# Performance work log

Measured on AMD Instinct MI355X. Metric: run time of the kernel, lower is better.

## Reference

```python
import jax, jax.numpy as jnp
import numpy as np

H = 23
Wd = 23
P = H * Wd            # 529 positions per 23x23 score map (hard-coded in the torch module)
B = 16384             # batch of score maps
TH = 0.05             # init kwarg peak_th
KS = 5                # init kwarg ks (max-pool kernel)
BN_EPS = 1e-5


def setup_inputs() -> dict:
    key = jax.random.key(0)
    k = jax.random.split(key, 18)
    def n(i, shape, scale=1.0):
        return scale * jax.random.normal(k[i], shape, dtype=jnp.float32)
    return {
        "target_scores": n(0, (2, B, P)),
        "anno_label": jax.random.uniform(k[1], (1, B, P), dtype=jnp.float32),
        # Conv1d(2->8, k=1) == Linear(2->8); BatchNorm1d in eval mode (running stats)
        "W1": n(2, (8, 2), 0.5), "b1": n(3, (8,), 0.1),
        "g1": 1.0 + n(4, (8,), 0.1), "be1": n(5, (8,), 0.1),
        "m1": n(6, (8,), 0.1), "v1": jax.random.uniform(k[7], (8,), minval=0.5, maxval=1.5),
        "W2": n(8, (8, 8), 0.3), "b2": n(9, (8,), 0.1),
        "g2": 1.0 + n(10, (8,), 0.1), "be2": n(11, (8,), 0.1),
        "m2": n(12, (8,), 0.1), "v2": jax.random.uniform(k[13], (8,), minval=0.5, maxval=1.5),
        "W3": n(14, (1, 8), 0.3), "b3": n(15, (1,), 0.1),
    }


def _find_peaks(scores_flat):
    """find_local_maxima: maxpool(ks, stride 1, pad ks//2) equality + threshold,
    then sort peaks by descending intensity per batch. Fixed-size padded version:
    returns coords [B,P,2] (float), sorted scores [B,P], valid mask [B,P]."""
    s = scores_flat.reshape(-1, H, Wd)
    smax = jax.lax.reduce_window(s, -jnp.inf, jax.lax.max, (1, KS, KS), (1, 1, 1), "SAME")
    mask = ((s == smax) & (s > TH)).reshape(-1, P)
    order = jnp.argsort(-jnp.where(mask, scores_flat, -jnp.inf), axis=1)
    sorted_s = jnp.take_along_axis(scores_flat, order, axis=1)
    valid = jnp.take_along_axis(mask, order, axis=1)
    coords = jnp.stack([(order // Wd).astype(jnp.float32),
                        (order % Wd).astype(jnp.float32)], axis=-1)
    return coords, sorted_s, valid


def _bn(x, g, b, m, v):
    return (x - m) * (g / jnp.sqrt(v + BN_EPS)) + b


def reference(target_scores, anno_label, W1, b1, g1, be1, m1, v1,
              W2, b2, g2, be2, m2, v2, W3, b3):
    scores_old = target_scores[0]            # [B,P]
    scores_cur = target_scores[1]            # [B,P]
    y_old = anno_label[0]                    # [B,P]

    c_old, s_old, val_old = _find_peaks(scores_old)
    c_cur, s_cur, val_cur = _find_peaks(scores_cur)

    # dcf.max2d(train_y_old): argmax coordinate of the training label
    gidx = jnp.argmax(y_old, axis=1)
    gc = jnp.stack([gidx // Wd, gidx % Wd], axis=-1).astype(jnp.float32)   # [B,2]

    # nearest old peak to the ground-truth coordinate
    d2 = jnp.sum((gc[:, None, :] - c_old) ** 2, axis=-1)
    d2 = jnp.where(val_old, d2, jnp.inf)
    pidx = jnp.argmin(d2, axis=1)
    cg = c_old[jnp.arange(c_old.shape[0]), pidx]                           # [B,2]

    # f_old = sum_j s_j * (cg - c_j) over valid old peaks
    sm_old = jnp.where(val_old, s_old, 0.0)
    f_old = jnp.sum(sm_old, axis=1)[:, None] * cg - jnp.einsum("bp,bpd->bd", sm_old, c_old)

    # f_cur[j] = sum_k s_k * (c_j - c_k)  (closed form of the pairwise sum)
    sm_cur = jnp.where(val_cur, s_cur, 0.0)
    S_cur = jnp.sum(sm_cur, axis=1)                                        # [B]
    M_cur = jnp.einsum("bp,bpd->bd", sm_cur, c_cur)                        # [B,2]
    f_cur = S_cur[:, None, None] * c_cur - M_cur[:, None, :]               # [B,P,2]

    diff2 = jnp.sum((f_old[:, None, :] - f_cur) ** 2, axis=-1)
    err = jnp.sqrt(jnp.maximum(diff2, 1e-24))                              # [B,P]

    feats = jnp.stack([err, s_cur], axis=-1)                               # [B,P,2]
    h = jax.nn.relu(_bn(feats @ W1.T + b1, g1, be1, m1, v1))
    h = jax.nn.relu(_bn(h @ W2.T + b2, g2, be2, m2, v2))
    pred = (h @ W3.T + b3)[..., 0]                                         # [B,P]
    pred = jnp.where(val_cur, pred, 0.0)  # only real peaks carry predictions
    return pred, c_cur, s_cur, val_cur
```

## Files before the change

kernel.cpp:

```cpp
#include <hip/hip_runtime.h>
#include <math.h>

#define H_   23
#define W_   23
#define P_   529
#define TH_  0.05f
#define NC   9
#define CAP  96
#define WPB  4
#define NTHR (WPB * 64)
#define WFLO (2 * P_ + 112)

#define WSYNC() do { asm volatile("" ::: "memory"); __builtin_amdgcn_wave_barrier(); } while (0)

__global__ __launch_bounds__(NTHR, 8) void peak_kernel(
    const float* __restrict__ tscores,
    const float* __restrict__ anno,
    const float* __restrict__ W1, const float* __restrict__ b1,
    const float* __restrict__ g1, const float* __restrict__ be1,
    const float* __restrict__ m1, const float* __restrict__ v1,
    const float* __restrict__ W2, const float* __restrict__ b2,
    const float* __restrict__ g2, const float* __restrict__ be2,
    const float* __restrict__ m2, const float* __restrict__ v2,
    const float* __restrict__ W3, const float* __restrict__ b3,
    float* __restrict__ out, int B)
{
    const int t  = threadIdx.x;
    const int l  = t & 63;
    const int wv = t >> 6;
    const int b  = blockIdx.x * WPB + wv;

    __shared__ float lds[WPB * WFLO];
    float* m  = lds + wv * WFLO;
    float* r  = m + P_;
    float* wt = r + P_;
    float* cs = r;
    int*   cp = (int*)(r + CAP);
    int*   rk = (int*)(r + 2*CAP);
    int*   ri = (int*)r;
    float* ps = wt;

    const unsigned long long ltm = (1ull << l) - 1ull;

    {
        int o = l >> 3;
        float sc2o = g2[o] / sqrtf(v2[o] + 1e-5f);
        wt[24 + l] = W2[l] * sc2o;
        if (l < 8) {
            float sc1 = g1[l] / sqrtf(v1[l] + 1e-5f);
            wt[2*l]     = W1[2*l] * sc1;
            wt[2*l + 1] = W1[2*l + 1] * sc1;
            wt[16 + l]  = (b1[l] - m1[l]) * sc1 + be1[l];
            float sc2 = g2[l] / sqrtf(v2[l] + 1e-5f);
            wt[88 + l]  = (b2[l] - m2[l]) * sc2 + be2[l];
            wt[96 + l]  = W3[l];
            if (l == 0) wt[104] = b3[0];
        }
    }

    const float* yrow = anno + (size_t)b * P_;
    const float* sold = tscores + (size_t)b * P_;
    const float* scur = tscores + (size_t)B * P_ + (size_t)b * P_;
    float ao[NC], so[NC], sc[NC];
    #pragma unroll
    for (int c = 0; c < NC; c++) { int p = 64*c + l; ao[c] = (p < P_) ? yrow[p] : -INFINITY; }
    #pragma unroll
    for (int c = 0; c < NC; c++) { int p = 64*c + l; so[c] = (p < P_) ? sold[p] : 0.f; }
    #pragma unroll
    for (int c = 0; c < NC; c++) { int p = 64*c + l; sc[c] = (p < P_) ? scur[p] : 0.f; }

    float bv = -INFINITY; int bi = 0x7fffffff;
    #pragma unroll
    for (int c = 0; c < NC; c++) {
        int p = 64*c + l;
        if (p < P_ && ao[c] > bv) { bv = ao[c]; bi = p; }
    }
    #pragma unroll
    for (int d = 32; d > 0; d >>= 1) {
        float ov = __shfl_xor(bv, d); int oi = __shfl_xor(bi, d);
        if (ov > bv || (ov == bv && oi < bi)) { bv = ov; bi = oi; }
    }
    const int gy = bi / W_, gx = bi - (bi / W_) * W_;

    #pragma unroll
    for (int c = 0; c < NC; c++) { int p = 64*c + l; if (p < P_) m[p] = so[c]; }
    WSYNC();
    #pragma unroll
    for (int c = 0; c < NC; c++) {
        int p = 64*c + l;
        if (p < P_) {
            int y = p / W_, x = p - y * W_;
            const float* row = &m[y * W_];
            float mx = row[x];
            if (x >= 1)      mx = fmaxf(mx, row[x-1]);
            if (x >= 2)      mx = fmaxf(mx, row[x-2]);
            if (x <= W_-2)   mx = fmaxf(mx, row[x+1]);
            if (x <= W_-3)   mx = fmaxf(mx, row[x+2]);
            r[p] = mx;
        }
    }
    WSYNC();
    float So = 0.f, Mor = 0.f, Moc = 0.f;
    float nd2 = INFINITY, ns = -INFINITY; int np = 0;
    #pragma unroll
    for (int c = 0; c < NC; c++) {
        int p = 64*c + l;
        if (p < P_) {
            int y = p / W_, x = p - y * W_;
            float s = so[c];
            float sm = r[p];
            if (y >= 1)    sm = fmaxf(sm, r[p - W_]);
            if (y >= 2)    sm = fmaxf(sm, r[p - 2*W_]);
            if (y <= H_-2) sm = fmaxf(sm, r[p + W_]);
            if (y <= H_-3) sm = fmaxf(sm, r[p + 2*W_]);
            if (s == sm && s > TH_) {
                So += s; Mor += s * (float)y; Moc += s * (float)x;
                int dy = gy - y, dx = gx - x;
                float d2 = (float)(dy*dy + dx*dx);
                if (d2 < nd2 || (d2 == nd2 && (s > ns || (s == ns && p < np)))) {
                    nd2 = d2; ns = s; np = p;
                }
            }
        }
    }
    #pragma unroll
    for (int d = 32; d > 0; d >>= 1) {
        So += __shfl_xor(So, d); Mor += __shfl_xor(Mor, d); Moc += __shfl_xor(Moc, d);
        float od2 = __shfl_xor(nd2, d), os = __shfl_xor(ns, d); int op = __shfl_xor(np, d);
        if (od2 < nd2 || (od2 == nd2 && (os > ns || (os == ns && op < np)))) {
            nd2 = od2; ns = os; np = op;
        }
    }
    const int cy = np / W_, cx = np - (np / W_) * W_;
    const float foldr = So * (float)cy - Mor;
    const float foldc = So * (float)cx - Moc;

    WSYNC();
    #pragma unroll
    for (int c = 0; c < NC; c++) { int p = 64*c + l; if (p < P_) m[p] = sc[c]; }
    WSYNC();
    #pragma unroll
    for (int c = 0; c < NC; c++) {
        int p = 64*c + l;
        if (p < P_) {
            int y = p / W_, x = p - y * W_;
            const float* row = &m[y * W_];
            float mx = row[x];
            if (x >= 1)      mx = fmaxf(mx, row[x-1]);
            if (x >= 2)      mx = fmaxf(mx, row[x-2]);
            if (x <= W_-2)   mx = fmaxf(mx, row[x+1]);
            if (x <= W_-3)   mx = fmaxf(mx, row[x+2]);
            r[p] = mx;
        }
    }
    WSYNC();
    float Sc = 0.f, Mcr = 0.f, Mcc = 0.f;
    int vb = 0;
    #pragma unroll
    for (int c = 0; c < NC; c++) {
        int p = 64*c + l;
        if (p < P_) {
            int y = p / W_, x = p - y * W_;
            float s = sc[c];
            float sm = r[p];
            if (y >= 1)    sm = fmaxf(sm, r[p - W_]);
            if (y >= 2)    sm = fmaxf(sm, r[p - 2*W_]);
            if (y <= H_-2) sm = fmaxf(sm, r[p + W_]);
            if (y <= H_-3) sm = fmaxf(sm, r[p + 2*W_]);
            if (s == sm && s > TH_) {
                vb |= 1 << c;
                Sc += s; Mcr += s * (float)y; Mcc += s * (float)x;
            }
        }
    }
    #pragma unroll
    for (int d = 32; d > 0; d >>= 1) {
        Sc += __shfl_xor(Sc, d); Mcr += __shfl_xor(Mcr, d); Mcc += __shfl_xor(Mcc, d);
    }
    WSYNC();

    int K = 0;
    int nb[NC];
    #pragma unroll
    for (int c = 0; c < NC; c++) {
        bool v = (vb >> c) & 1;
        unsigned long long bt = __ballot(v);
        int my = K + __popcll(bt & ltm);
        nb[c] = my;
        if (v && my < CAP) { cs[my] = sc[c]; cp[my] = 64*c + l; }
        K += __popcll(bt);
    }
    WSYNC();

    const int Kc = K > CAP ? CAP : K;
    for (int i = l; i < Kc; i += 64) {
        float si = cs[i]; int pi = cp[i]; int rr = 0;
        for (int j = 0; j < Kc; j++) {
            float sj = cs[j]; int pj = cp[j];
            rr += (sj > si || (sj == si && pj < pi)) ? 1 : 0;
        }
        rk[i] = rr;
    }
    WSYNC();

    auto mlp = [&](int i, float& pv, int& rko) {
        int p = cp[i];
        float s = cs[i];
        rko = rk[i];
        int y = p / W_, x = p - (p / W_) * W_;
        float fcr = Sc * (float)y - Mcr;
        float fcc = Sc * (float)x - Mcc;
        float dr = foldr - fcr, dc = foldc - fcc;
        float err = sqrtf(fmaxf(dr*dr + dc*dc, 1e-24f));
        float h1[8];
        #pragma unroll
        for (int o = 0; o < 8; o++)
            h1[o] = fmaxf(fmaf(err, wt[2*o], fmaf(s, wt[2*o+1], wt[16+o])), 0.f);
        float pred = wt[104];
        #pragma unroll
        for (int o = 0; o < 8; o++) {
            float z = wt[88 + o];
            #pragma unroll
            for (int i2 = 0; i2 < 8; i2++) z = fmaf(h1[i2], wt[24 + o*8 + i2], z);
            pred = fmaf(fmaxf(z, 0.f), wt[96 + o], pred);
        }
        pv = pred;
    };
    float pv0 = 0.f, pv1 = 0.f; int rk0 = -1, rk1 = -1;
    if (l < Kc)      mlp(l, pv0, rk0);
    if (64 + l < Kc) mlp(64 + l, pv1, rk1);
    WSYNC();
    if (rk0 >= 0 && rk0 < CAP) ps[rk0] = pv0;
    if (rk1 >= 0 && rk1 < CAP) ps[rk1] = pv1;

    int slot[NC];
    #pragma unroll
    for (int c = 0; c < NC; c++) {
        int p = 64*c + l;
        if (p < P_) {
            bool v = (vb >> c) & 1;
            int n = nb[c];
            slot[c] = v ? ((n < CAP) ? rk[n] : n) : (K + p - n);
        }
    }
    WSYNC();
    #pragma unroll
    for (int c = 0; c < NC; c++) {
        int p = 64*c + l;
        if (p < P_) ri[slot[c]] = p;
    }
    WSYNC();

    const size_t BP = (size_t)B * P_;
    float* out_pred = out;
    float* out_c    = out + BP;
    float* out_s    = out + 3 * BP;
    float* out_v    = out + 4 * BP;
    const size_t rowbase = (size_t)b * P_;

    #pragma unroll
    for (int c = 0; c < NC; c++) {
        int j = 64*c + l;
        if (j < P_) {
            int p = ri[j];
            int y = p / W_, x = p - (p / W_) * W_;
            bool val = j < K;
            float pv = (val && j < CAP) ? ps[j] : 0.f;
            float s  = m[p];
            out_pred[rowbase + j] = pv;
            ((float2*)out_c)[rowbase + j] = make_float2((float)y, (float)x);
            out_s[rowbase + j] = s;
            out_v[rowbase + j] = val ? 1.f : 0.f;
        }
    }
}

extern "C" void kernel_launch(void* const* d_in, const int* in_sizes, int n_in,
                              void* d_out, int out_size, void* d_ws, size_t ws_size,
                              hipStream_t stream) {
    const int B = in_sizes[0] / (2 * P_);
    hipLaunchKernelGGL(peak_kernel, dim3((B + WPB - 1) / WPB), dim3(NTHR), 0, stream,
        (const float*)d_in[0], (const float*)d_in[1],
        (const float*)d_in[2], (const float*)d_in[3], (const float*)d_in[4],
        (const float*)d_in[5], (const float*)d_in[6], (const float*)d_in[7],
        (const float*)d_in[8], (const float*)d_in[9], (const float*)d_in[10],
        (const float*)d_in[11], (const float*)d_in[12], (const float*)d_in[13],
        (const float*)d_in[14], (const float*)d_in[15],
        (float*)d_out, B);
}
```

Measured before the change: 71.37 us.

## Pad max-pool staging with -inf borders, precompute folded MLP weights, nontemporal stores

```diff
diff --git a/kernel.cpp b/kernel.cpp
--- a/kernel.cpp
+++ b/kernel.cpp
@@ -9,13 +9,13 @@
 #define CAP  96
 #define WPB  4
 #define NTHR (WPB * 64)
-#define WFLO (2 * P_ + 112)
+#define WFLO 1248
+
+typedef float f2_t __attribute__((ext_vector_type(2)));
 
 #define WSYNC() do { asm volatile("" ::: "memory"); __builtin_amdgcn_wave_barrier(); } while (0)
 
-__global__ __launch_bounds__(NTHR, 8) void peak_kernel(
-    const float* __restrict__ tscores,
-    const float* __restrict__ anno,
+__global__ __launch_bounds__(64) void fold_kernel(
     const float* __restrict__ W1, const float* __restrict__ b1,
     const float* __restrict__ g1, const float* __restrict__ be1,
     const float* __restrict__ m1, const float* __restrict__ v1,
@@ -23,38 +23,56 @@
     const float* __restrict__ g2, const float* __restrict__ be2,
     const float* __restrict__ m2, const float* __restrict__ v2,
     const float* __restrict__ W3, const float* __restrict__ b3,
+    float* __restrict__ wf)
+{
+    const int l = threadIdx.x;
+    {
+        int o = l >> 3;
+        wf[24 + l] = W2[l] * (g2[o] / sqrtf(v2[o] + 1e-5f));
+    }
+    if (l < 8) {
+        float sc1 = g1[l] / sqrtf(v1[l] + 1e-5f);
+        wf[2*l]     = W1[2*l] * sc1;
+        wf[2*l + 1] = W1[2*l + 1] * sc1;
+        wf[16 + l]  = (b1[l] - m1[l]) * sc1 + be1[l];
+        float sc2 = g2[l] / sqrtf(v2[l] + 1e-5f);
+        wf[88 + l]  = (b2[l] - m2[l]) * sc2 + be2[l];
+        wf[96 + l]  = W3[l];
+        if (l == 0) wf[104] = b3[0];
+    }
+}
+
+__global__ __launch_bounds__(NTHR, 8) void peak_kernel(
+    const float* __restrict__ tscores,
+    const float* __restrict__ anno,
+    const float* __restrict__ wf,
     float* __restrict__ out, int B)
 {
     const int t  = threadIdx.x;
     const int l  = t & 63;
     const int wv = t >> 6;
     const int b  = blockIdx.x * WPB + wv;
+    if (b >= B) return;
 
     __shared__ float lds[WPB * WFLO];
-    float* m  = lds + wv * WFLO;
-    float* r  = m + P_;
-    float* wt = r + P_;
-    float* cs = r;
-    int*   cp = (int*)(r + CAP);
-    int*   rk = (int*)(r + 2*CAP);
-    int*   ri = (int*)r;
-    float* ps = wt;
+    float* m27 = lds + wv * WFLO;
+    float* r27 = m27 + 621;
+    float* cs  = r27;
+    int*   cp  = (int*)(r27 + CAP);
+    int*   rk  = (int*)(r27 + 2*CAP);
+    int*   ri  = (int*)r27;
+    float* ps  = r27 + 529;
 
     const unsigned long long ltm = (1ull << l) - 1ull;
 
-    {
-        int o = l >> 3;
-        float sc2o = g2[o] / sqrtf(v2[o] + 1e-5f);
-        wt[24 + l] = W2[l] * sc2o;
-        if (l < 8) {
-            float sc1 = g1[l] / sqrtf(v1[l] + 1e-5f);
-            wt[2*l]     = W1[2*l] * sc1;
-            wt[2*l + 1] = W1[2*l + 1] * sc1;
-            wt[16 + l]  = (b1[l] - m1[l]) * sc1 + be1[l];
-            float sc2 = g2[l] / sqrtf(v2[l] + 1e-5f);
-            wt[88 + l]  = (b2[l] - m2[l]) * sc2 + be2[l];
-            wt[96 + l]  = W3[l];
-            if (l == 0) wt[104] = b3[0];
+    #pragma unroll
+    for (int k0 = 0; k0 < 2; k0++) {
+        int k = 64 * k0 + l;
+        if (k < 92) {
+            int rw = k >> 2, csel = k & 3;
+            m27[rw * 27 + csel + (csel >= 2 ? 23 : 0)] = -INFINITY;
+            int rsel = k / 23, col = k - 23 * (k / 23);
+            r27[(rsel + (rsel >= 2 ? 23 : 0)) * 23 + col] = -INFINITY;
         }
     }
 
@@ -69,6 +87,14 @@
     #pragma unroll
     for (int c = 0; c < NC; c++) { int p = 64*c + l; sc[c] = (p < P_) ? scur[p] : 0.f; }
 
+    int yy[NC], xx[NC];
+    #pragma unroll
+    for (int c = 0; c < NC; c++) {
+        int p = 64*c + l;
+        yy[c] = p / W_;
+        xx[c] = p - yy[c] * W_;
+    }
+
     float bv = -INFINITY; int bi = 0x7fffffff;
     #pragma unroll
     for (int c = 0; c < NC; c++) {
@@ -82,23 +108,34 @@
     }
     const int gy = bi / W_, gx = bi - (bi / W_) * W_;
 
-    #pragma unroll
-    for (int c = 0; c < NC; c++) { int p = 64*c + l; if (p < P_) m[p] = so[c]; }
-    WSYNC();
-    #pragma unroll
-    for (int c = 0; c < NC; c++) {
-        int p = 64*c + l;
-        if (p < P_) {
-            int y = p / W_, x = p - y * W_;
-            const float* row = &m[y * W_];
-            float mx = row[x];
-            if (x >= 1)      mx = fmaxf(mx, row[x-1]);
-            if (x >= 2)      mx = fmaxf(mx, row[x-2]);
-            if (x <= W_-2)   mx = fmaxf(mx, row[x+1]);
-            if (x <= W_-3)   mx = fmaxf(mx, row[x+2]);
-            r[p] = mx;
-        }
-    }
+    auto stage = [&](const float* v) {
+        #pragma unroll
+        for (int c = 0; c < NC; c++) {
+            int p = 64*c + l;
+            if (p < P_) m27[p + 4*yy[c] + 2] = v[c];
+        }
+    };
+    auto rowmax = [&]() {
+        #pragma unroll
+        for (int c = 0; c < NC; c++) {
+            int p = 64*c + l;
+            if (p < P_) {
+                const float* bp = &m27[p + 4*yy[c]];
+                float t0 = bp[0], t1 = bp[1], t2 = bp[2], t3 = bp[3], t4 = bp[4];
+                r27[p + 46] = fmaxf(fmaxf(fmaxf(t0, t1), fmaxf(t2, t3)), t4);
+            }
+        }
+    };
+    auto colmax = [&](int c) {
+        int p = 64*c + l;
+        const float* bp = &r27[p];
+        float t0 = bp[0], t1 = bp[23], t2 = bp[46], t3 = bp[69], t4 = bp[92];
+        return fmaxf(fmaxf(fmaxf(t0, t1), fmaxf(t2, t3)), t4);
+    };
+
+    stage(so);
+    WSYNC();
+    rowmax();
     WSYNC();
     float So = 0.f, Mor = 0.f, Moc = 0.f;
     float nd2 = INFINITY, ns = -INFINITY; int np = 0;
@@ -106,16 +143,12 @@
     for (int c = 0; c < NC; c++) {
         int p = 64*c + l;
         if (p < P_) {
-            int y = p / W_, x = p - y * W_;
             float s = so[c];
-            float sm = r[p];
-            if (y >= 1)    sm = fmaxf(sm, r[p - W_]);
-            if (y >= 2)    sm = fmaxf(sm, r[p - 2*W_]);
-            if (y <= H_-2) sm = fmaxf(sm, r[p + W_]);
-            if (y <= H_-3) sm = fmaxf(sm, r[p + 2*W_]);
+            float sm = colmax(c);
             if (s == sm && s > TH_) {
-                So += s; Mor += s * (float)y; Moc += s * (float)x;
-                int dy = gy - y, dx = gx - x;
+                float fy = (float)yy[c], fx = (float)xx[c];
+                So += s; Mor += s * fy; Moc += s * fx;
+                int dy = gy - yy[c], dx = gx - xx[c];
                 float d2 = (float)(dy*dy + dx*dx);
                 if (d2 < nd2 || (d2 == nd2 && (s > ns || (s == ns && p < np)))) {
                     nd2 = d2; ns = s; np = p;
@@ -136,23 +169,9 @@
     const float foldc = So * (float)cx - Moc;
 
     WSYNC();
-    #pragma unroll
-    for (int c = 0; c < NC; c++) { int p = 64*c + l; if (p < P_) m[p] = sc[c]; }
-    WSYNC();
-    #pragma unroll
-    for (int c = 0; c < NC; c++) {
-        int p = 64*c + l;
-        if (p < P_) {
-            int y = p / W_, x = p - y * W_;
-            const float* row = &m[y * W_];
-            float mx = row[x];
-            if (x >= 1)      mx = fmaxf(mx, row[x-1]);
-            if (x >= 2)      mx = fmaxf(mx, row[x-2]);
-            if (x <= W_-2)   mx = fmaxf(mx, row[x+1]);
-            if (x <= W_-3)   mx = fmaxf(mx, row[x+2]);
-            r[p] = mx;
-        }
-    }
+    stage(sc);
+    WSYNC();
+    rowmax();
     WSYNC();
     float Sc = 0.f, Mcr = 0.f, Mcc = 0.f;
     int vb = 0;
@@ -160,16 +179,11 @@
     for (int c = 0; c < NC; c++) {
         int p = 64*c + l;
         if (p < P_) {
-            int y = p / W_, x = p - y * W_;
             float s = sc[c];
-            float sm = r[p];
-            if (y >= 1)    sm = fmaxf(sm, r[p - W_]);
-            if (y >= 2)    sm = fmaxf(sm, r[p - 2*W_]);
-            if (y <= H_-2) sm = fmaxf(sm, r[p + W_]);
-            if (y <= H_-3) sm = fmaxf(sm, r[p + 2*W_]);
+            float sm = colmax(c);
             if (s == sm && s > TH_) {
                 vb |= 1 << c;
-                Sc += s; Mcr += s * (float)y; Mcc += s * (float)x;
+                Sc += s; Mcr += s * (float)yy[c]; Mcc += s * (float)xx[c];
             }
         }
     }
@@ -215,23 +229,22 @@
         float h1[8];
         #pragma unroll
         for (int o = 0; o < 8; o++)
-            h1[o] = fmaxf(fmaf(err, wt[2*o], fmaf(s, wt[2*o+1], wt[16+o])), 0.f);
-        float pred = wt[104];
+            h1[o] = fmaxf(fmaf(err, wf[2*o], fmaf(s, wf[2*o+1], wf[16+o])), 0.f);
+        float pred = wf[104];
         #pragma unroll
         for (int o = 0; o < 8; o++) {
-            float z = wt[88 + o];
+            float z = wf[88 + o];
             #pragma unroll
-            for (int i2 = 0; i2 < 8; i2++) z = fmaf(h1[i2], wt[24 + o*8 + i2], z);
-            pred = fmaf(fmaxf(z, 0.f), wt[96 + o], pred);
+            for (int i2 = 0; i2 < 8; i2++) z = fmaf(h1[i2], wf[24 + o*8 + i2], z);
+            pred = fmaf(fmaxf(z, 0.f), wf[96 + o], pred);
         }
         pv = pred;
     };
     float pv0 = 0.f, pv1 = 0.f; int rk0 = -1, rk1 = -1;
     if (l < Kc)      mlp(l, pv0, rk0);
     if (64 + l < Kc) mlp(64 + l, pv1, rk1);
-    WSYNC();
-    if (rk0 >= 0 && rk0 < CAP) ps[rk0] = pv0;
-    if (rk1 >= 0 && rk1 < CAP) ps[rk1] = pv1;
+    if (rk0 >= 0) ps[rk0] = pv0;
+    if (rk1 >= 0) ps[rk1] = pv1;
 
     int slot[NC];
     #pragma unroll
@@ -266,11 +279,12 @@
             int y = p / W_, x = p - (p / W_) * W_;
             bool val = j < K;
             float pv = (val && j < CAP) ? ps[j] : 0.f;
-            float s  = m[p];
-            out_pred[rowbase + j] = pv;
-            ((float2*)out_c)[rowbase + j] = make_float2((float)y, (float)x);
-            out_s[rowbase + j] = s;
-            out_v[rowbase + j] = val ? 1.f : 0.f;
+            float s  = m27[p + 4*y + 2];
+            f2_t co; co.x = (float)y; co.y = (float)x;
+            __builtin_nontemporal_store(pv, &out_pred[rowbase + j]);
+            __builtin_nontemporal_store(co, &((f2_t*)out_c)[rowbase + j]);
+            __builtin_nontemporal_store(s, &out_s[rowbase + j]);
+            __builtin_nontemporal_store(val ? 1.f : 0.f, &out_v[rowbase + j]);
         }
     }
 }
@@ -279,12 +293,14 @@
                               void* d_out, int out_size, void* d_ws, size_t ws_size,
                               hipStream_t stream) {
     const int B = in_sizes[0] / (2 * P_);
-    hipLaunchKernelGGL(peak_kernel, dim3((B + WPB - 1) / WPB), dim3(NTHR), 0, stream,
-        (const float*)d_in[0], (const float*)d_in[1],
+    float* wf = (float*)d_ws;
+    hipLaunchKernelGGL(fold_kernel, dim3(1), dim3(64), 0, stream,
         (const float*)d_in[2], (const float*)d_in[3], (const float*)d_in[4],
         (const float*)d_in[5], (const float*)d_in[6], (const float*)d_in[7],
         (const float*)d_in[8], (const float*)d_in[9], (const float*)d_in[10],
         (const float*)d_in[11], (const float*)d_in[12], (const float*)d_in[13],
-        (const float*)d_in[14], (const float*)d_in[15],
+        (const float*)d_in[14], (const float*)d_in[15], wf);
+    hipLaunchKernelGGL(peak_kernel, dim3((B + WPB - 1) / WPB), dim3(NTHR), 0, stream,
+        (const float*)d_in[0], (const float*)d_in[1], (const float*)wf,
         (float*)d_out, B);
 }
```

Result: slower. 106.3 us (+48.9%).

## Process two positions per lane with vectorized loads and direct global row-max

Applied to the files above, without the earlier changes.

```diff
diff --git a/kernel.cpp b/kernel.cpp
--- a/kernel.cpp
+++ b/kernel.cpp
@@ -6,10 +6,14 @@
 #define P_   529
 #define TH_  0.05f
 #define NC   9
+#define PC   5
 #define CAP  96
 #define WPB  4
 #define NTHR (WPB * 64)
-#define WFLO (2 * P_ + 112)
+#define WFLO 1176
+
+typedef float f2_t  __attribute__((ext_vector_type(2)));
+typedef float f2u_t __attribute__((ext_vector_type(2), aligned(4)));
 
 #define WSYNC() do { asm volatile("" ::: "memory"); __builtin_amdgcn_wave_barrier(); } while (0)
 
@@ -29,11 +33,12 @@
     const int l  = t & 63;
     const int wv = t >> 6;
     const int b  = blockIdx.x * WPB + wv;
+    if (b >= B) return;
 
     __shared__ float lds[WPB * WFLO];
-    float* m  = lds + wv * WFLO;
-    float* r  = m + P_;
-    float* wt = r + P_;
+    float* r  = lds + wv * WFLO;
+    float* m  = r + 532;
+    float* wt = r + 1064;
     float* cs = r;
     int*   cp = (int*)(r + CAP);
     int*   rk = (int*)(r + 2*CAP);
@@ -61,14 +66,10 @@
     const float* yrow = anno + (size_t)b * P_;
     const float* sold = tscores + (size_t)b * P_;
     const float* scur = tscores + (size_t)B * P_ + (size_t)b * P_;
-    float ao[NC], so[NC], sc[NC];
+
+    float ao[NC];
     #pragma unroll
     for (int c = 0; c < NC; c++) { int p = 64*c + l; ao[c] = (p < P_) ? yrow[p] : -INFINITY; }
-    #pragma unroll
-    for (int c = 0; c < NC; c++) { int p = 64*c + l; so[c] = (p < P_) ? sold[p] : 0.f; }
-    #pragma unroll
-    for (int c = 0; c < NC; c++) { int p = 64*c + l; sc[c] = (p < P_) ? scur[p] : 0.f; }
-
     float bv = -INFINITY; int bi = 0x7fffffff;
     #pragma unroll
     for (int c = 0; c < NC; c++) {
@@ -82,43 +83,83 @@
     }
     const int gy = bi / W_, gx = bi - (bi / W_) * W_;
 
-    #pragma unroll
-    for (int c = 0; c < NC; c++) { int p = 64*c + l; if (p < P_) m[p] = so[c]; }
-    WSYNC();
-    #pragma unroll
-    for (int c = 0; c < NC; c++) {
-        int p = 64*c + l;
-        if (p < P_) {
-            int y = p / W_, x = p - y * W_;
-            const float* row = &m[y * W_];
-            float mx = row[x];
-            if (x >= 1)      mx = fmaxf(mx, row[x-1]);
-            if (x >= 2)      mx = fmaxf(mx, row[x-2]);
-            if (x <= W_-2)   mx = fmaxf(mx, row[x+1]);
-            if (x <= W_-3)   mx = fmaxf(mx, row[x+2]);
-            r[p] = mx;
-        }
-    }
+    auto rmpass = [&](const float* __restrict__ src, f2_t* bv2, bool stm) {
+        #pragma unroll
+        for (int c = 0; c < PC; c++) {
+            int q = 128*c + 2*l;
+            f2_t z; z.x = 0.f; z.y = 0.f; bv2[c] = z;
+            if (q < P_) {
+                int y0 = q / W_, x0 = q - y0 * W_;
+                f2_t bq = *(const f2u_t*)(src + q);
+                f2_t aq = bq, cq = bq;
+                if (q >= 2)     aq = *(const f2u_t*)(src + q - 2);
+                if (q + 2 < P_) cq = *(const f2u_t*)(src + q + 2);
+                bool wrap = (x0 == W_ - 1);
+                float rm0 = bq.x;
+                if (x0 >= 1)  rm0 = fmaxf(rm0, aq.y);
+                if (x0 >= 2)  rm0 = fmaxf(rm0, aq.x);
+                if (x0 <= 21) rm0 = fmaxf(rm0, bq.y);
+                if (x0 <= 20) rm0 = fmaxf(rm0, cq.x);
+                float rm1 = bq.y;
+                if (!wrap)             rm1 = fmaxf(rm1, bq.x);
+                if (!wrap && x0 >= 1)  rm1 = fmaxf(rm1, aq.y);
+                if (wrap || x0 <= 20)  rm1 = fmaxf(rm1, cq.x);
+                if (wrap || x0 <= 19)  rm1 = fmaxf(rm1, cq.y);
+                f2_t rmv; rmv.x = rm0; rmv.y = rm1;
+                *(f2_t*)(r + q) = rmv;
+                if (stm) *(f2_t*)(m + q) = bq;
+                bv2[c] = bq;
+            }
+        }
+    };
+    auto colwin = [&](int q, f2_t* v) {
+        v[0] = *(const f2_t*)(r + q - 46);
+        v[1] = *(const f2u_t*)(r + q - 23);
+        v[2] = *(const f2_t*)(r + q);
+        v[3] = *(const f2u_t*)(r + q + 23);
+        v[4] = *(const f2_t*)(r + q + 46);
+    };
+
+    f2_t bo[PC];
+    rmpass(sold, bo, false);
     WSYNC();
     float So = 0.f, Mor = 0.f, Moc = 0.f;
     float nd2 = INFINITY, ns = -INFINITY; int np = 0;
     #pragma unroll
-    for (int c = 0; c < NC; c++) {
-        int p = 64*c + l;
-        if (p < P_) {
-            int y = p / W_, x = p - y * W_;
-            float s = so[c];
-            float sm = r[p];
-            if (y >= 1)    sm = fmaxf(sm, r[p - W_]);
-            if (y >= 2)    sm = fmaxf(sm, r[p - 2*W_]);
-            if (y <= H_-2) sm = fmaxf(sm, r[p + W_]);
-            if (y <= H_-3) sm = fmaxf(sm, r[p + 2*W_]);
-            if (s == sm && s > TH_) {
-                So += s; Mor += s * (float)y; Moc += s * (float)x;
-                int dy = gy - y, dx = gx - x;
+    for (int c = 0; c < PC; c++) {
+        int q = 128*c + 2*l;
+        if (q < P_) {
+            int y0 = q / W_, x0 = q - y0 * W_;
+            bool wrap = (x0 == W_ - 1);
+            int y1 = y0 + (wrap ? 1 : 0);
+            f2_t v[5];
+            colwin(q, v);
+            float sm0 = v[2].x;
+            if (y0 >= 1)  sm0 = fmaxf(sm0, v[1].x);
+            if (y0 >= 2)  sm0 = fmaxf(sm0, v[0].x);
+            if (y0 <= 21) sm0 = fmaxf(sm0, v[3].x);
+            if (y0 <= 20) sm0 = fmaxf(sm0, v[4].x);
+            float sm1 = v[2].y;
+            if (y1 >= 1)  sm1 = fmaxf(sm1, v[1].y);
+            if (y1 >= 2)  sm1 = fmaxf(sm1, v[0].y);
+            if (y1 <= 21) sm1 = fmaxf(sm1, v[3].y);
+            if (y1 <= 20) sm1 = fmaxf(sm1, v[4].y);
+            float s0 = bo[c].x, s1 = bo[c].y;
+            if (s0 == sm0 && s0 > TH_) {
+                So += s0; Mor += s0 * (float)y0; Moc += s0 * (float)x0;
+                int dy = gy - y0, dx = gx - x0;
                 float d2 = (float)(dy*dy + dx*dx);
-                if (d2 < nd2 || (d2 == nd2 && (s > ns || (s == ns && p < np)))) {
-                    nd2 = d2; ns = s; np = p;
+                if (d2 < nd2 || (d2 == nd2 && (s0 > ns || (s0 == ns && q < np)))) {
+                    nd2 = d2; ns = s0; np = q;
+                }
+            }
+            if (q + 1 < P_ && s1 == sm1 && s1 > TH_) {
+                int x1 = wrap ? 0 : x0 + 1;
+                So += s1; Mor += s1 * (float)y1; Moc += s1 * (float)x1;
+                int dy = gy - y1, dx = gx - x1;
+                float d2 = (float)(dy*dy + dx*dx);
+                if (d2 < nd2 || (d2 == nd2 && (s1 > ns || (s1 == ns && q+1 < np)))) {
+                    nd2 = d2; ns = s1; np = q + 1;
                 }
             }
         }
@@ -136,40 +177,39 @@
     const float foldc = So * (float)cx - Moc;
 
     WSYNC();
-    #pragma unroll
-    for (int c = 0; c < NC; c++) { int p = 64*c + l; if (p < P_) m[p] = sc[c]; }
-    WSYNC();
-    #pragma unroll
-    for (int c = 0; c < NC; c++) {
-        int p = 64*c + l;
-        if (p < P_) {
-            int y = p / W_, x = p - y * W_;
-            const float* row = &m[y * W_];
-            float mx = row[x];
-            if (x >= 1)      mx = fmaxf(mx, row[x-1]);
-            if (x >= 2)      mx = fmaxf(mx, row[x-2]);
-            if (x <= W_-2)   mx = fmaxf(mx, row[x+1]);
-            if (x <= W_-3)   mx = fmaxf(mx, row[x+2]);
-            r[p] = mx;
-        }
-    }
+    f2_t bc[PC];
+    rmpass(scur, bc, true);
     WSYNC();
     float Sc = 0.f, Mcr = 0.f, Mcc = 0.f;
-    int vb = 0;
-    #pragma unroll
-    for (int c = 0; c < NC; c++) {
-        int p = 64*c + l;
-        if (p < P_) {
-            int y = p / W_, x = p - y * W_;
-            float s = sc[c];
-            float sm = r[p];
-            if (y >= 1)    sm = fmaxf(sm, r[p - W_]);
-            if (y >= 2)    sm = fmaxf(sm, r[p - 2*W_]);
-            if (y <= H_-2) sm = fmaxf(sm, r[p + W_]);
-            if (y <= H_-3) sm = fmaxf(sm, r[p + 2*W_]);
-            if (s == sm && s > TH_) {
-                vb |= 1 << c;
-                Sc += s; Mcr += s * (float)y; Mcc += s * (float)x;
+    int vb0 = 0, vb1 = 0;
+    #pragma unroll
+    for (int c = 0; c < PC; c++) {
+        int q = 128*c + 2*l;
+        if (q < P_) {
+            int y0 = q / W_, x0 = q - y0 * W_;
+            bool wrap = (x0 == W_ - 1);
+            int y1 = y0 + (wrap ? 1 : 0);
+            f2_t v[5];
+            colwin(q, v);
+            float sm0 = v[2].x;
+            if (y0 >= 1)  sm0 = fmaxf(sm0, v[1].x);
+            if (y0 >= 2)  sm0 = fmaxf(sm0, v[0].x);
+            if (y0 <= 21) sm0 = fmaxf(sm0, v[3].x);
+            if (y0 <= 20) sm0 = fmaxf(sm0, v[4].x);
+            float sm1 = v[2].y;
+            if (y1 >= 1)  sm1 = fmaxf(sm1, v[1].y);
+            if (y1 >= 2)  sm1 = fmaxf(sm1, v[0].y);
+            if (y1 <= 21) sm1 = fmaxf(sm1, v[3].y);
+            if (y1 <= 20) sm1 = fmaxf(sm1, v[4].y);
+            float s0 = bc[c].x, s1 = bc[c].y;
+            if (s0 == sm0 && s0 > TH_) {
+                vb0 |= 1 << c;
+                Sc += s0; Mcr += s0 * (float)y0; Mcc += s0 * (float)x0;
+            }
+            if (q + 1 < P_ && s1 == sm1 && s1 > TH_) {
+                vb1 |= 1 << c;
+                int x1 = wrap ? 0 : x0 + 1;
+                Sc += s1; Mcr += s1 * (float)y1; Mcc += s1 * (float)x1;
             }
         }
     }
@@ -180,15 +220,18 @@
     WSYNC();
 
     int K = 0;
-    int nb[NC];
-    #pragma unroll
-    for (int c = 0; c < NC; c++) {
-        bool v = (vb >> c) & 1;
-        unsigned long long bt = __ballot(v);
-        int my = K + __popcll(bt & ltm);
-        nb[c] = my;
-        if (v && my < CAP) { cs[my] = sc[c]; cp[my] = 64*c + l; }
-        K += __popcll(bt);
+    int nbp[PC];
+    #pragma unroll
+    for (int c = 0; c < PC; c++) {
+        bool v0 = (vb0 >> c) & 1, v1 = (vb1 >> c) & 1;
+        unsigned long long bt0 = __ballot(v0), bt1 = __ballot(v1);
+        int before = K + __popcll(bt0 & ltm) + __popcll(bt1 & ltm);
+        nbp[c] = before;
+        int q = 128*c + 2*l;
+        if (v0 && before < CAP) { cs[before] = bc[c].x; cp[before] = q; }
+        int my1 = before + (v0 ? 1 : 0);
+        if (v1 && my1 < CAP)    { cs[my1] = bc[c].y;    cp[my1] = q + 1; }
+        K += __popcll(bt0) + __popcll(bt1);
     }
     WSYNC();
 
@@ -230,24 +273,25 @@
     if (l < Kc)      mlp(l, pv0, rk0);
     if (64 + l < Kc) mlp(64 + l, pv1, rk1);
     WSYNC();
-    if (rk0 >= 0 && rk0 < CAP) ps[rk0] = pv0;
-    if (rk1 >= 0 && rk1 < CAP) ps[rk1] = pv1;
-
-    int slot[NC];
-    #pragma unroll
-    for (int c = 0; c < NC; c++) {
-        int p = 64*c + l;
-        if (p < P_) {
-            bool v = (vb >> c) & 1;
-            int n = nb[c];
-            slot[c] = v ? ((n < CAP) ? rk[n] : n) : (K + p - n);
-        }
-    }
-    WSYNC();
-    #pragma unroll
-    for (int c = 0; c < NC; c++) {
-        int p = 64*c + l;
-        if (p < P_) ri[slot[c]] = p;
+    if (rk0 >= 0) ps[rk0] = pv0;
+    if (rk1 >= 0) ps[rk1] = pv1;
+
+    int sl0[PC], sl1[PC];
+    #pragma unroll
+    for (int c = 0; c < PC; c++) {
+        int q = 128*c + 2*l;
+        bool v0 = (vb0 >> c) & 1, v1 = (vb1 >> c) & 1;
+        int nb0 = nbp[c];
+        int nb1 = nb0 + (v0 ? 1 : 0);
+        if (v0) sl0[c] = (nb0 < CAP) ? rk[nb0] : nb0; else sl0[c] = K + q - nb0;
+        if (v1) sl1[c] = (nb1 < CAP) ? rk[nb1] : nb1; else sl1[c] = K + (q + 1) - nb1;
+    }
+    WSYNC();
+    #pragma unroll
+    for (int c = 0; c < PC; c++) {
+        int q = 128*c + 2*l;
+        if (q < P_)     ri[sl0[c]] = q;
+        if (q + 1 < P_) ri[sl1[c]] = q + 1;
     }
     WSYNC();
 
@@ -267,8 +311,9 @@
             bool val = j < K;
             float pv = (val && j < CAP) ? ps[j] : 0.f;
             float s  = m[p];
+            f2_t co; co.x = (float)y; co.y = (float)x;
             out_pred[rowbase + j] = pv;
-            ((float2*)out_c)[rowbase + j] = make_float2((float)y, (float)x);
+            ((f2_t*)out_c)[rowbase + j] = co;
             out_s[rowbase + j] = s;
             out_v[rowbase + j] = val ? 1.f : 0.f;
         }
```

Measured after the change: 89.51 us. 1.25x slower.
